# Kernel optimization log

Hardware: AMD Instinct MI355X
Metric: run time of the kernel (lower is better)

The kernel has to match this reference:

```python
import jax, jax.numpy as jnp
import numpy as np

N_NODES = 100000
N_EDGES = 1600000
D_IN = 128
D_OUT = 128


def setup_inputs() -> dict:
    key = jax.random.key(0)
    k1, k2, k3, k4, k5 = jax.random.split(key, 5)
    x = jax.random.normal(k1, (N_NODES, D_IN), dtype=jnp.float32)
    x_0 = jax.random.normal(k2, (N_NODES, D_IN), dtype=jnp.float32)
    edge_index = jax.random.randint(k3, (2, N_EDGES), 0, N_NODES, dtype=jnp.int64)
    # GCNConv linear weight (glorot-ish scale) and bias
    W = jax.random.normal(k4, (D_IN, D_OUT), dtype=jnp.float32) / np.sqrt(D_IN)
    b = jax.random.normal(k5, (D_OUT,), dtype=jnp.float32) * 0.01
    return {"x": x, "x_0": x_0, "W": W, "b": b, "edge_index": edge_index}


def reference(x, x_0, W, b, edge_index):
    # SemiGCNConv.forward: relu(GCNConv(x, edge_index)); x_0 is unused.
    N = x.shape[0]
    # GCNConv default: add self-loops, symmetric normalization
    loop = jnp.arange(N, dtype=edge_index.dtype)
    src = jnp.concatenate([edge_index[0], loop])  # [E+N]
    dst = jnp.concatenate([edge_index[1], loop])  # [E+N]
    # degree of target nodes (edge_weight = 1)
    deg = jax.ops.segment_sum(jnp.ones_like(dst, dtype=x.dtype), dst, num_segments=N)
    deg_inv_sqrt = jnp.where(deg > 0, jax.lax.rsqrt(deg), 0.0)
    norm = deg_inv_sqrt[src] * deg_inv_sqrt[dst]  # [E+N]
    # linear transform first (PyG order), then normalized scatter-add aggregation
    h = x @ W  # [N, D_OUT]
    msg = h[src] * norm[:, None]  # gather + scale, [E+N, D_OUT]
    out = jax.ops.segment_sum(msg, dst, num_segments=N) + b
    return jax.nn.relu(out)
```

## Files before the change

kernel.cpp:

```cpp
#include <hip/hip_runtime.h>

#define N_NODES 100000
#define N_EDGES 1600000
#define D 128
#define G 256
#define NB 391
#define NB_PAD 392
#define CAP 6144
#define SUBCAP 1536
#define EPT 4

typedef __attribute__((ext_vector_type(8))) short bf16x8;
typedef __attribute__((ext_vector_type(4))) float f32x4;

__device__ inline float bf2f(unsigned short u) {
    return __uint_as_float(((unsigned int)u) << 16);
}
__device__ inline unsigned short f2bf(float f) {
    unsigned int u = __float_as_uint(f);
    unsigned int r = u + 0x7FFF + ((u >> 16) & 1);
    return (unsigned short)(r >> 16);
}

__device__ inline int wave_incl_scan(int v, int lane) {
    #pragma unroll
    for (int off = 1; off < 64; off <<= 1) {
        int y = __shfl_up(v, off);
        if (lane >= off) v += y;
    }
    return v;
}

__global__ __launch_bounds__(256) void bin_count(const int* __restrict__ ei,
                                                 int* __restrict__ gcursor,
                                                 unsigned int* __restrict__ bins) {
    __shared__ int hist[NB];
    __shared__ int base[NB];
    const int tid = threadIdx.x;
    for (int i = tid; i < NB; i += 256) hist[i] = 0;
    __syncthreads();

    const long long e0 = (long long)blockIdx.x * (256 * EPT) + (long long)tid * EPT;
    const bool active = (e0 < N_EDGES);
    unsigned int packed[EPT]; int bkt[EPT]; int rnk[EPT];
    if (active) {
        int4 s = *(const int4*)(ei + e0);
        int4 d = *(const int4*)(ei + N_EDGES + e0);
        bkt[0] = d.x >> 8; packed[0] = (unsigned)s.x | ((unsigned)(d.x & 255) << 17);
        bkt[1] = d.y >> 8; packed[1] = (unsigned)s.y | ((unsigned)(d.y & 255) << 17);
        bkt[2] = d.z >> 8; packed[2] = (unsigned)s.z | ((unsigned)(d.z & 255) << 17);
        bkt[3] = d.w >> 8; packed[3] = (unsigned)s.w | ((unsigned)(d.w & 255) << 17);
        #pragma unroll
        for (int j = 0; j < EPT; ++j) rnk[j] = atomicAdd(&hist[bkt[j]], 1);
    }
    __syncthreads();
    for (int i = tid; i < NB; i += 256) {
        int c = hist[i];
        base[i] = c ? atomicAdd(&gcursor[i], c) : 0;
    }
    __syncthreads();
    if (active) {
        #pragma unroll
        for (int j = 0; j < EPT; ++j) {
            int pos = base[bkt[j]] + rnk[j];
            if (pos < CAP) bins[(size_t)bkt[j] * CAP + pos] = packed[j];
        }
    }
}

__global__ __launch_bounds__(256) void deg_bins(const unsigned int* __restrict__ bins,
                                                const int* __restrict__ gcursor,
                                                int* __restrict__ deg) {
    __shared__ int degL[G];
    const int b = blockIdx.x, t = threadIdx.x;
    degL[t] = 0;
    __syncthreads();
    int cb = gcursor[b];
    if (cb > CAP) cb = CAP;
    const unsigned int* mybins = bins + (size_t)b * CAP;
    for (int i = t; i < cb; i += 256)
        atomicAdd(&degL[(mybins[i] >> 17) & 255], 1);
    __syncthreads();
    int node = b * G + t;
    if (node < N_NODES) deg[node] = degL[t];
}

__global__ __launch_bounds__(512) void gemm_h_mfma(
        const float* __restrict__ x, const float* __restrict__ W,
        const int* __restrict__ deg, unsigned short* __restrict__ h) {
    __shared__ unsigned short wt[D * D];
    const int tid  = threadIdx.x;
    const int lane = tid & 63;
    const int wv   = tid >> 6;
    const int rb   = blockIdx.x * 128 + wv * 16;

    int arow = rb + (lane & 15);
    if (arow >= N_NODES) arow = N_NODES - 1;
    const float4* xrow = (const float4*)(x + (size_t)arow * D);
    float4 af[8];
    #pragma unroll
    for (int kt = 0; kt < 4; ++kt) {
        int fi = kt * 8 + (lane >> 4) * 2;
        af[kt * 2]     = xrow[fi];
        af[kt * 2 + 1] = xrow[fi + 1];
    }

    const float4* W4 = (const float4*)W;
    float4 wreg[8];
    #pragma unroll
    for (int i = 0; i < 8; ++i) wreg[i] = W4[tid + 512 * i];
    #pragma unroll
    for (int i = 0; i < 8; ++i) {
        int idx = tid + 512 * i;
        int k  = idx >> 5;
        int c0 = (idx & 31) * 4;
        float v[4] = {wreg[i].x, wreg[i].y, wreg[i].z, wreg[i].w};
        #pragma unroll
        for (int j = 0; j < 4; ++j) {
            int c = c0 + j;
            int byte = (c * 256 + k * 2) ^ ((c & 7) << 4);
            *(unsigned short*)((char*)wt + byte) = f2bf(v[j]);
        }
    }
    __syncthreads();

    bf16x8 a[4];
    #pragma unroll
    for (int kt = 0; kt < 4; ++kt) {
        float4 u = af[kt * 2], v = af[kt * 2 + 1];
        a[kt][0] = (short)f2bf(u.x); a[kt][1] = (short)f2bf(u.y);
        a[kt][2] = (short)f2bf(u.z); a[kt][3] = (short)f2bf(u.w);
        a[kt][4] = (short)f2bf(v.x); a[kt][5] = (short)f2bf(v.y);
        a[kt][6] = (short)f2bf(v.z); a[kt][7] = (short)f2bf(v.w);
    }

    f32x4 acc[8];
    #pragma unroll
    for (int ct = 0; ct < 8; ++ct) acc[ct] = (f32x4){0.f, 0.f, 0.f, 0.f};

    const int cbase = lane & 15;
    const int kgrp  = (lane >> 4) * 8;
    #pragma unroll
    for (int ct = 0; ct < 8; ++ct) {
        int c = ct * 16 + cbase;
        #pragma unroll
        for (int kt = 0; kt < 4; ++kt) {
            int byte = (c * 256 + (kt * 32 + kgrp) * 2) ^ ((c & 7) << 4);
            bf16x8 bfr = *(const bf16x8*)((const char*)wt + byte);
            acc[ct] = __builtin_amdgcn_mfma_f32_16x16x32_bf16(a[kt], bfr, acc[ct], 0, 0, 0);
        }
    }

    float dq[4]; int orow[4];
    #pragma unroll
    for (int q = 0; q < 4; ++q) {
        orow[q] = rb + (lane >> 4) * 4 + q;
        int rr = orow[q] < N_NODES ? orow[q] : 0;
        dq[q] = rsqrtf((float)deg[rr] + 1.0f);
    }
    #pragma unroll
    for (int ct = 0; ct < 8; ++ct) {
        int col = ct * 16 + (lane & 15);
        #pragma unroll
        for (int q = 0; q < 4; ++q) {
            if (orow[q] < N_NODES)
                h[(size_t)orow[q] * D + col] = f2bf(acc[ct][q] * dq[q]);
        }
    }
}

__global__ __launch_bounds__(256) void bucket_gather(const unsigned int* __restrict__ bins,
                                                     const int* __restrict__ gcursor,
                                                     const ushort4* __restrict__ h4,
                                                     const float4* __restrict__ b4,
                                                     float4* __restrict__ out4) {
    __shared__ int degL[64];
    __shared__ int rsL[64];
    __shared__ int curL[64];
    __shared__ int csrL[SUBCAP];
    const int j = blockIdx.x, t = threadIdx.x;
    const int b = j >> 2, q = j & 3;
    int cb = gcursor[b];
    if (cb > CAP) cb = CAP;
    if (t < 64) { degL[t] = 0; curL[t] = 0; }
    __syncthreads();
    const unsigned int* mybins = bins + (size_t)b * CAP;
    for (int i = t; i < cb; i += 256) {
        unsigned int u = mybins[i];
        if (((u >> 23) & 3) == (unsigned)q)
            atomicAdd(&degL[(u >> 17) & 63], 1);
    }
    __syncthreads();
    if (t < 64) {
        int v = degL[t];
        int incl = wave_incl_scan(v, t);
        rsL[t] = incl - v;
    }
    __syncthreads();
    for (int i = t; i < cb; i += 256) {
        unsigned int u = mybins[i];
        if (((u >> 23) & 3) == (unsigned)q) {
            int dl = (u >> 17) & 63;
            int pos = rsL[dl] + atomicAdd(&curL[dl], 1);
            if (pos < SUBCAP) csrL[pos] = (int)(u & 0x1FFFF);
        }
    }
    __syncthreads();

    const int c = t & 31, g = t >> 5;
    for (int nl = g; nl < 64; nl += 8) {
        int node = j * 64 + nl;
        if (node >= N_NODES) break;
        int rs = rsL[nl], dg = degL[nl];
        ushort4 hv = h4[(size_t)node * 32 + c];
        float4 acc = {bf2f(hv.x), bf2f(hv.y), bf2f(hv.z), bf2f(hv.w)};
        int jj = 0;
        for (; jj + 4 <= dg; jj += 4) {
            int s0 = csrL[rs + jj],     s1 = csrL[rs + jj + 1];
            int s2 = csrL[rs + jj + 2], s3 = csrL[rs + jj + 3];
            ushort4 v0 = h4[(size_t)s0 * 32 + c];
            ushort4 v1 = h4[(size_t)s1 * 32 + c];
            ushort4 v2 = h4[(size_t)s2 * 32 + c];
            ushort4 v3 = h4[(size_t)s3 * 32 + c];
            acc.x += bf2f(v0.x) + bf2f(v1.x) + bf2f(v2.x) + bf2f(v3.x);
            acc.y += bf2f(v0.y) + bf2f(v1.y) + bf2f(v2.y) + bf2f(v3.y);
            acc.z += bf2f(v0.z) + bf2f(v1.z) + bf2f(v2.z) + bf2f(v3.z);
            acc.w += bf2f(v0.w) + bf2f(v1.w) + bf2f(v2.w) + bf2f(v3.w);
        }
        for (; jj < dg; ++jj) {
            int s = csrL[rs + jj];
            ushort4 v = h4[(size_t)s * 32 + c];
            acc.x += bf2f(v.x); acc.y += bf2f(v.y);
            acc.z += bf2f(v.z); acc.w += bf2f(v.w);
        }
        float dn = rsqrtf((float)dg + 1.0f);
        float4 bb = b4[c];
        float4 o;
        o.x = fmaxf(fmaf(dn, acc.x, bb.x), 0.f);
        o.y = fmaxf(fmaf(dn, acc.y, bb.y), 0.f);
        o.z = fmaxf(fmaf(dn, acc.z, bb.z), 0.f);
        o.w = fmaxf(fmaf(dn, acc.w, bb.w), 0.f);
        out4[(size_t)node * 32 + c] = o;
    }
}

extern "C" void kernel_launch(void* const* d_in, const int* in_sizes, int n_in,
                              void* d_out, int out_size, void* d_ws, size_t ws_size,
                              hipStream_t stream) {
    const float* x  = (const float*)d_in[0];
    const float* W  = (const float*)d_in[2];
    const float* b  = (const float*)d_in[3];
    const int*   ei = (const int*)d_in[4];
    float* out = (float*)d_out;

    unsigned short* h  = (unsigned short*)d_ws;
    int*   deg         = (int*)(h + (size_t)N_NODES * D);
    int*   gcursor     = deg + N_NODES;
    unsigned int* bins = (unsigned int*)(gcursor + NB_PAD);

    hipMemsetAsync(gcursor, 0, NB_PAD * sizeof(int), stream);

    bin_count<<<(N_EDGES + 256 * EPT - 1) / (256 * EPT), 256, 0, stream>>>(ei, gcursor, bins);
    deg_bins<<<NB, 256, 0, stream>>>(bins, gcursor, deg);
    gemm_h_mfma<<<(N_NODES + 127) / 128, 512, 0, stream>>>(x, W, deg, h);
    bucket_gather<<<NB * 4, 256, 0, stream>>>(bins, gcursor, (const ushort4*)h,
                                              (const float4*)b, (float4*)out);
}
```

Baseline: 283.3 us.

## Pad bin reservations to 16, raise edges per thread, split gather into eighths

bin_count now handles 16 edges per thread and reserves global bin space in multiples of 16, so there are fewer global atomics per bucket. The unused slots are filled with a sentinel by a full memset of the bins buffer, and the downstream kernels skip it. bucket_gather splits each 256-node bucket into 8 sub-blocks of 32 nodes instead of 4 of 64, which doubles the grid for more parallelism. The cost is an extra memset of about 12.8 MB, each gather block rescanning the whole bucket (8x redundant reads instead of 4x), and a higher CAP to absorb the padding.

Measured after the change: 278.1 us. Within noise of the previous version (-1.8%).

```diff
diff --git a/kernel.cpp b/kernel.cpp
--- a/kernel.cpp
+++ b/kernel.cpp
@@ -6,9 +6,10 @@
 #define G 256
 #define NB 391
 #define NB_PAD 392
-#define CAP 6144
-#define SUBCAP 1536
-#define EPT 4
+#define CAP 8192
+#define SUBCAP 768
+#define EPT 16
+#define SENT 0xFFFFFFFFu
 
 typedef __attribute__((ext_vector_type(8))) short bf16x8;
 typedef __attribute__((ext_vector_type(4))) float f32x4;
@@ -44,19 +45,25 @@
     const bool active = (e0 < N_EDGES);
     unsigned int packed[EPT]; int bkt[EPT]; int rnk[EPT];
     if (active) {
-        int4 s = *(const int4*)(ei + e0);
-        int4 d = *(const int4*)(ei + N_EDGES + e0);
-        bkt[0] = d.x >> 8; packed[0] = (unsigned)s.x | ((unsigned)(d.x & 255) << 17);
-        bkt[1] = d.y >> 8; packed[1] = (unsigned)s.y | ((unsigned)(d.y & 255) << 17);
-        bkt[2] = d.z >> 8; packed[2] = (unsigned)s.z | ((unsigned)(d.z & 255) << 17);
-        bkt[3] = d.w >> 8; packed[3] = (unsigned)s.w | ((unsigned)(d.w & 255) << 17);
+        const int4* s4 = (const int4*)(ei + e0);
+        const int4* d4 = (const int4*)(ei + N_EDGES + e0);
+        #pragma unroll
+        for (int q = 0; q < EPT / 4; ++q) {
+            int4 s = s4[q], d = d4[q];
+            int j = q * 4;
+            bkt[j+0] = d.x >> 8; packed[j+0] = (unsigned)s.x | ((unsigned)(d.x & 255) << 17);
+            bkt[j+1] = d.y >> 8; packed[j+1] = (unsigned)s.y | ((unsigned)(d.y & 255) << 17);
+            bkt[j+2] = d.z >> 8; packed[j+2] = (unsigned)s.z | ((unsigned)(d.z & 255) << 17);
+            bkt[j+3] = d.w >> 8; packed[j+3] = (unsigned)s.w | ((unsigned)(d.w & 255) << 17);
+        }
         #pragma unroll
         for (int j = 0; j < EPT; ++j) rnk[j] = atomicAdd(&hist[bkt[j]], 1);
     }
     __syncthreads();
     for (int i = tid; i < NB; i += 256) {
         int c = hist[i];
-        base[i] = c ? atomicAdd(&gcursor[i], c) : 0;
+        int cpad = (c + 15) & ~15;
+        base[i] = cpad ? atomicAdd(&gcursor[i], cpad) : 0;
     }
     __syncthreads();
     if (active) {
@@ -78,8 +85,10 @@
     int cb = gcursor[b];
     if (cb > CAP) cb = CAP;
     const unsigned int* mybins = bins + (size_t)b * CAP;
-    for (int i = t; i < cb; i += 256)
-        atomicAdd(&degL[(mybins[i] >> 17) & 255], 1);
+    for (int i = t; i < cb; i += 256) {
+        unsigned int u = mybins[i];
+        if (u != SENT) atomicAdd(&degL[(u >> 17) & 255], 1);
+    }
     __syncthreads();
     int node = b * G + t;
     if (node < N_NODES) deg[node] = degL[t];
@@ -174,24 +183,25 @@
                                                      const ushort4* __restrict__ h4,
                                                      const float4* __restrict__ b4,
                                                      float4* __restrict__ out4) {
-    __shared__ int degL[64];
-    __shared__ int rsL[64];
-    __shared__ int curL[64];
+    __shared__ int degL[32];
+    __shared__ int rsL[32];
+    __shared__ int curL[32];
     __shared__ int csrL[SUBCAP];
     const int j = blockIdx.x, t = threadIdx.x;
-    const int b = j >> 2, q = j & 3;
+    const int b = j >> 3;
+    const unsigned int q = (unsigned)(j & 7);
     int cb = gcursor[b];
     if (cb > CAP) cb = CAP;
-    if (t < 64) { degL[t] = 0; curL[t] = 0; }
+    if (t < 32) { degL[t] = 0; curL[t] = 0; }
     __syncthreads();
     const unsigned int* mybins = bins + (size_t)b * CAP;
     for (int i = t; i < cb; i += 256) {
         unsigned int u = mybins[i];
-        if (((u >> 23) & 3) == (unsigned)q)
-            atomicAdd(&degL[(u >> 17) & 63], 1);
-    }
-    __syncthreads();
-    if (t < 64) {
+        if (u != SENT && ((u >> 22) & 7) == q)
+            atomicAdd(&degL[(u >> 17) & 31], 1);
+    }
+    __syncthreads();
+    if (t < 32) {
         int v = degL[t];
         int incl = wave_incl_scan(v, t);
         rsL[t] = incl - v;
@@ -199,8 +209,8 @@
     __syncthreads();
     for (int i = t; i < cb; i += 256) {
         unsigned int u = mybins[i];
-        if (((u >> 23) & 3) == (unsigned)q) {
-            int dl = (u >> 17) & 63;
+        if (u != SENT && ((u >> 22) & 7) == q) {
+            int dl = (u >> 17) & 31;
             int pos = rsL[dl] + atomicAdd(&curL[dl], 1);
             if (pos < SUBCAP) csrL[pos] = (int)(u & 0x1FFFF);
         }
@@ -208,8 +218,8 @@
     __syncthreads();
 
     const int c = t & 31, g = t >> 5;
-    for (int nl = g; nl < 64; nl += 8) {
-        int node = j * 64 + nl;
+    for (int nl = g; nl < 32; nl += 8) {
+        int node = b * G + (int)q * 32 + nl;
         if (node >= N_NODES) break;
         int rs = rsL[nl], dg = degL[nl];
         ushort4 hv = h4[(size_t)node * 32 + c];
@@ -259,10 +269,11 @@
     unsigned int* bins = (unsigned int*)(gcursor + NB_PAD);
 
     hipMemsetAsync(gcursor, 0, NB_PAD * sizeof(int), stream);
+    hipMemsetAsync(bins, 0xFF, (size_t)NB * CAP * sizeof(unsigned int), stream);
 
     bin_count<<<(N_EDGES + 256 * EPT - 1) / (256 * EPT), 256, 0, stream>>>(ei, gcursor, bins);
     deg_bins<<<NB, 256, 0, stream>>>(bins, gcursor, deg);
     gemm_h_mfma<<<(N_NODES + 127) / 128, 512, 0, stream>>>(x, W, deg, h);
-    bucket_gather<<<NB * 4, 256, 0, stream>>>(bins, gcursor, (const ushort4*)h,
+    bucket_gather<<<NB * 8, 256, 0, stream>>>(bins, gcursor, (const ushort4*)h,
                                               (const float4*)b, (float4*)out);
 }
```
